# Optimization experiments

Measured on AMD Instinct MI355X. Metric: run time of the kernel, lower is better.

## Reference

```python
import jax, jax.numpy as jnp
import numpy as np

N_HEAD = 16

def setup_inputs() -> dict:
    key = jax.random.key(0)
    ks = jax.random.split(key, 5)
    B, S, C = 4, 2048, 1024
    x = jax.random.normal(ks[0], (B, S, C), dtype=jnp.float32)
    w_qkv = jax.random.normal(ks[1], (C, 3 * C), dtype=jnp.float32) * (1.0 / np.sqrt(C))
    b_qkv = jnp.zeros((3 * C,), dtype=jnp.float32)
    w_proj = jax.random.normal(ks[2], (C, C), dtype=jnp.float32) * (1.0 / np.sqrt(C))
    b_proj = jnp.zeros((C,), dtype=jnp.float32)
    return {"x": x, "w_qkv": w_qkv, "b_qkv": b_qkv, "w_proj": w_proj, "b_proj": b_proj}

def reference(x, w_qkv, b_qkv, w_proj, b_proj):
    B, S, C = x.shape
    H = N_HEAD
    D = C // H
    qkv = x @ w_qkv + b_qkv                       # [B,S,3C]
    q, k, v = jnp.split(qkv, 3, axis=-1)
    # [B,S,C] -> [B,H,S,D]
    q = q.reshape(B, S, H, D).transpose(0, 2, 1, 3)
    k = k.reshape(B, S, H, D).transpose(0, 2, 1, 3)
    v = v.reshape(B, S, H, D).transpose(0, 2, 1, 3)
    scores = jnp.einsum('bhqd,bhkd->bhqk', q, k) / jnp.sqrt(jnp.float32(D))
    causal = jnp.tril(jnp.ones((S, S), dtype=bool))
    scores = jnp.where(causal[None, None], scores, -jnp.inf)
    weights = jax.nn.softmax(scores, axis=-1)     # dropout p=0 -> identity
    out = jnp.einsum('bhqk,bhkd->bhqd', weights, v)
    out = out.transpose(0, 2, 1, 3).reshape(B, S, C)
    return out @ w_proj + b_proj
```

## Files before the change

### kernel.cpp

```cpp
#include <hip/hip_runtime.h>

#define SDIM 2048
#define CDIM 1024
#define BDIM 4
#define HDIM 16
#define DDIM 64

#define ATT_SCALE 0.18033688011112042f

typedef __attribute__((ext_vector_type(8))) short bf16x8;
typedef __attribute__((ext_vector_type(4))) short bf16x4;
typedef __attribute__((ext_vector_type(4))) float f32x4;
typedef unsigned short u16;

#define MFMA __builtin_amdgcn_mfma_f32_16x16x32_bf16
#define LDS_ORDER_FENCE() __asm__ __volatile__("" ::: "memory")

__device__ __forceinline__ u16 f2b(float f) {
    union { float f; unsigned u; } v; v.f = f;
    unsigned r = v.u + 0x7FFFu + ((v.u >> 16) & 1u);
    return (u16)(r >> 16);
}
__device__ __forceinline__ u16 f2b_trunc(float f) {
    union { float f; unsigned u; } v; v.f = f;
    return (u16)(v.u >> 16);
}

typedef const __attribute__((address_space(1))) unsigned int* gas_t;
typedef __attribute__((address_space(3))) unsigned int* las_t;
__device__ __forceinline__ void cp16(const void* g, void* l) {
    __builtin_amdgcn_global_load_lds((gas_t)g, (las_t)l, 16, 0, 0);
}

__device__ __forceinline__ float fast_exp2(float x) {
#if __has_builtin(__builtin_amdgcn_exp2f)
    return __builtin_amdgcn_exp2f(x);
#else
    return __exp2f(x);
#endif
}

__global__ __launch_bounds__(256) void prep(
    const float* __restrict__ x, const float* __restrict__ w_qkv,
    const float* __restrict__ w_proj,
    u16* __restrict__ Xb, u16* __restrict__ WqT, u16* __restrict__ WpT)
{
    __shared__ __align__(16) u16 t[64][72];
    const int bx = blockIdx.x;
    const int tid = threadIdx.x;

    if (bx < 4096) {
        int i = (bx * 256 + tid) * 8;
        float4 a = *reinterpret_cast<const float4*>(&x[i]);
        float4 b = *reinterpret_cast<const float4*>(&x[i + 4]);
        u16 u[8];
        u[0]=f2b(a.x); u[1]=f2b(a.y); u[2]=f2b(a.z); u[3]=f2b(a.w);
        u[4]=f2b(b.x); u[5]=f2b(b.y); u[6]=f2b(b.z); u[7]=f2b(b.w);
        *reinterpret_cast<uint4*>(&Xb[i]) = *reinterpret_cast<uint4*>(u);
        return;
    }

    const float* src; u16* dst; int N, n0, k0;
    if (bx < 4096 + 768) {
        int b2 = bx - 4096;
        src = w_qkv; dst = WqT; N = 3 * CDIM;
        n0 = (b2 % 48) * 64; k0 = (b2 / 48) * 64;
    } else {
        int b2 = bx - 4864;
        src = w_proj; dst = WpT; N = CDIM;
        n0 = (b2 % 16) * 64; k0 = (b2 / 16) * 64;
    }
    const int K = CDIM;
#pragma unroll
    for (int it = 0; it < 4; it++) {
        int c = tid + it * 256;
        int r = c >> 4, c4 = (c & 15) * 4;
        float4 f = *reinterpret_cast<const float4*>(&src[(size_t)(k0 + r) * N + n0 + c4]);
        t[c4 + 0][r] = f2b(f.x);
        t[c4 + 1][r] = f2b(f.y);
        t[c4 + 2][r] = f2b(f.z);
        t[c4 + 3][r] = f2b(f.w);
    }
    __syncthreads();
#pragma unroll
    for (int it = 0; it < 2; it++) {
        int c = tid + it * 256;
        int r = c >> 3, c8 = (c & 7) * 8;
        *reinterpret_cast<uint4*>(&dst[(size_t)(n0 + r) * K + k0 + c8]) =
            *reinterpret_cast<const uint4*>(&t[r][c8]);
    }
}


#define PHASE_TAIL()                                                          \
    LDS_ORDER_FENCE();                                                        \
    __builtin_amdgcn_s_barrier();                                             \
    __asm__ __volatile__("s_waitcnt lgkmcnt(0)" ::: "memory");                \
    __builtin_amdgcn_sched_barrier(0)

#define PHASE_END()                                                           \
    LDS_ORDER_FENCE();                                                        \
    __builtin_amdgcn_s_barrier()

__global__ __launch_bounds__(512, 2) void gemm_qkv(
    const u16* __restrict__ A, const u16* __restrict__ Bt,
    const float* __restrict__ bias,
    u16* __restrict__ Qb, u16* __restrict__ Kb, u16* __restrict__ Vtb)
{
    __shared__ __align__(16) u16 smem[3 * 16384 + 3 * 8192];
    u16* const AsAll = smem;
    u16* const BsAll = smem + 3 * 16384;

    const int tid = threadIdx.x, lane = tid & 63, wave = tid >> 6;
    const int wm = wave >> 1, wn = wave & 1;
    const int l16 = lane & 15, quad = lane >> 4;
    const int bid = blockIdx.x;
    const int w = (bid & 7) * 96 + (bid >> 3);
    const int bx = w % 24, by = w / 24;
    const int m0 = by * 256, n0 = bx * 128;
    const int K = CDIM;

    const int l8 = lane & 7, lr = lane >> 3;
    const int sg = l8 ^ lr;
    const int arow = wave * 8 + lr;

#define STG_A(sb, k0, s)  cp16(&A [(size_t)(m0 + (s) * 64 + arow) * K + (k0) + sg * 8], \
                               &AsAll[(sb) * 16384 + ((s) * 512 + wave * 64) * 8])
#define STG_B(sb, k0, s)  cp16(&Bt[(size_t)(n0 + (s) * 64 + arow) * K + (k0) + sg * 8], \
                               &BsAll[(sb) * 8192 + ((s) * 512 + wave * 64) * 8])
#define FRA(i, kk) (*reinterpret_cast<const bf16x8*>(                                   \
        &AsB[((wm * 64 + (i) * 16 + l16) * 8 + (((kk) * 4 + quad) ^ (l16 & 7))) * 8]))
#define FRB(j, kk) (*reinterpret_cast<const bf16x8*>(                                   \
        &BsB[((wn * 64 + (j) * 16 + l16) * 8 + (((kk) * 4 + quad) ^ (l16 & 7))) * 8]))

    f32x4 acc[4][4];
#pragma unroll
    for (int i = 0; i < 4; i++)
#pragma unroll
        for (int j = 0; j < 4; j++) acc[i][j] = (f32x4){0.f, 0.f, 0.f, 0.f};

    const int NT = K / 64;
    STG_A(0, 0, 0); STG_A(0, 0, 1); STG_A(0, 0, 2); STG_A(0, 0, 3);
    STG_B(0, 0, 0); STG_B(0, 0, 1);
    STG_A(1, 64, 0); STG_A(1, 64, 1); STG_A(1, 64, 2); STG_A(1, 64, 3);
    STG_B(1, 64, 0); STG_B(1, 64, 1);
    __asm__ __volatile__("s_waitcnt vmcnt(6)" ::: "memory");
    __builtin_amdgcn_s_barrier();
    LDS_ORDER_FENCE();

    for (int t = 0; t < NT; t++) {
        const int buf = t % 3, sbuf = (t + 2) % 3;
        const int kst = (t + 2) * 64;
        const bool st = (t + 2) < NT;
        const u16* AsB = &AsAll[buf * 16384];
        const u16* BsB = &BsAll[buf * 8192];

        bf16x8 b0, b1, b2, b3, a0, a1;

        b0 = FRB(0, 0); b1 = FRB(1, 0); b2 = FRB(2, 0); b3 = FRB(3, 0);
        a0 = FRA(0, 0); a1 = FRA(1, 0);
        if (st) { STG_A(sbuf, kst, 0); STG_A(sbuf, kst, 1); }
        PHASE_TAIL();
        __builtin_amdgcn_s_setprio(1);
        acc[0][0] = MFMA(a0, b0, acc[0][0], 0, 0, 0);
        acc[0][1] = MFMA(a0, b1, acc[0][1], 0, 0, 0);
        acc[0][2] = MFMA(a0, b2, acc[0][2], 0, 0, 0);
        acc[0][3] = MFMA(a0, b3, acc[0][3], 0, 0, 0);
        acc[1][0] = MFMA(a1, b0, acc[1][0], 0, 0, 0);
        acc[1][1] = MFMA(a1, b1, acc[1][1], 0, 0, 0);
        acc[1][2] = MFMA(a1, b2, acc[1][2], 0, 0, 0);
        acc[1][3] = MFMA(a1, b3, acc[1][3], 0, 0, 0);
        __builtin_amdgcn_s_setprio(0);
        PHASE_END();

        a0 = FRA(2, 0); a1 = FRA(3, 0);
        if (st) { STG_A(sbuf, kst, 2); STG_A(sbuf, kst, 3); }
        PHASE_TAIL();
        __builtin_amdgcn_s_setprio(1);
        acc[2][0] = MFMA(a0, b0, acc[2][0], 0, 0, 0);
        acc[2][1] = MFMA(a0, b1, acc[2][1], 0, 0, 0);
        acc[2][2] = MFMA(a0, b2, acc[2][2], 0, 0, 0);
        acc[2][3] = MFMA(a0, b3, acc[2][3], 0, 0, 0);
        acc[3][0] = MFMA(a1, b0, acc[3][0], 0, 0, 0);
        acc[3][1] = MFMA(a1, b1, acc[3][1], 0, 0, 0);
        acc[3][2] = MFMA(a1, b2, acc[3][2], 0, 0, 0);
        acc[3][3] = MFMA(a1, b3, acc[3][3], 0, 0, 0);
        __builtin_amdgcn_s_setprio(0);
        PHASE_END();

        b0 = FRB(0, 1); b1 = FRB(1, 1); b2 = FRB(2, 1); b3 = FRB(3, 1);
        a0 = FRA(0, 1); a1 = FRA(1, 1);
        if (st) { STG_B(sbuf, kst, 0); STG_B(sbuf, kst, 1); }
        PHASE_TAIL();
        __builtin_amdgcn_s_setprio(1);
        acc[0][0] = MFMA(a0, b0, acc[0][0], 0, 0, 0);
        acc[0][1] = MFMA(a0, b1, acc[0][1], 0, 0, 0);
        acc[0][2] = MFMA(a0, b2, acc[0][2], 0, 0, 0);
        acc[0][3] = MFMA(a0, b3, acc[0][3], 0, 0, 0);
        acc[1][0] = MFMA(a1, b0, acc[1][0], 0, 0, 0);
        acc[1][1] = MFMA(a1, b1, acc[1][1], 0, 0, 0);
        acc[1][2] = MFMA(a1, b2, acc[1][2], 0, 0, 0);
        acc[1][3] = MFMA(a1, b3, acc[1][3], 0, 0, 0);
        __builtin_amdgcn_s_setprio(0);
        PHASE_END();

        a0 = FRA(2, 1); a1 = FRA(3, 1);
        PHASE_TAIL();
        __builtin_amdgcn_s_setprio(1);
        acc[2][0] = MFMA(a0, b0, acc[2][0], 0, 0, 0);
        acc[2][1] = MFMA(a0, b1, acc[2][1], 0, 0, 0);
        acc[2][2] = MFMA(a0, b2, acc[2][2], 0, 0, 0);
        acc[2][3] = MFMA(a0, b3, acc[2][3], 0, 0, 0);
        acc[3][0] = MFMA(a1, b0, acc[3][0], 0, 0, 0);
        acc[3][1] = MFMA(a1, b1, acc[3][1], 0, 0, 0);
        acc[3][2] = MFMA(a1, b2, acc[3][2], 0, 0, 0);
        acc[3][3] = MFMA(a1, b3, acc[3][3], 0, 0, 0);
        __builtin_amdgcn_s_setprio(0);
        if (t < NT - 2) {
            __asm__ __volatile__("s_waitcnt vmcnt(6)" ::: "memory");
        } else if (t == NT - 2) {
            __asm__ __volatile__("s_waitcnt vmcnt(0)" ::: "memory");
        }
        PHASE_END();
    }
#undef STG_A
#undef STG_B
#undef FRA
#undef FRB

    const int mm0 = m0 + wm * 64;
    const int bidx = mm0 >> 11, s0 = mm0 & 2047;
    const int n_base = n0 + wn * 64;
    u16* eb = &smem[wave * (16 * 68)];
    const int erow = lane >> 2, ec = (lane & 3) * 16;

    if (n0 >= 2 * CDIM) {
        const int h = (n_base - 2 * CDIM) >> 6;
        const size_t gb = ((size_t)(bidx * HDIM + h)) * DDIM * SDIM;
#pragma unroll
        for (int j = 0; j < 4; j++) {
            float bvj = bias[n_base + j * 16 + l16];
            LDS_ORDER_FENCE();
#pragma unroll
            for (int i = 0; i < 4; i++)
#pragma unroll
                for (int r = 0; r < 4; r++)
                    eb[l16 * 68 + i * 16 + quad * 4 + r] = f2b(acc[i][j][r] + bvj);
            LDS_ORDER_FENCE();
            union { bf16x4 hp[4]; uint4 u[2]; } pk;
            pk.hp[0] = *reinterpret_cast<const bf16x4*>(&eb[erow * 68 + ec]);
            pk.hp[1] = *reinterpret_cast<const bf16x4*>(&eb[erow * 68 + ec + 4]);
            pk.hp[2] = *reinterpret_cast<const bf16x4*>(&eb[erow * 68 + ec + 8]);
            pk.hp[3] = *reinterpret_cast<const bf16x4*>(&eb[erow * 68 + ec + 12]);
            u16* gp = &Vtb[gb + (size_t)(j * 16 + erow) * SDIM + s0 + ec];
            *reinterpret_cast<uint4*>(gp)     = pk.u[0];
            *reinterpret_cast<uint4*>(gp + 8) = pk.u[1];
        }
    } else {
        const bool isK = (n_base >= CDIM);
        u16* dst = isK ? Kb : Qb;
        const float scale = isK ? 1.0f : ATT_SCALE;
        const int hh = (n_base & 1023) >> 6;
        const size_t hb = ((size_t)(bidx * HDIM + hh)) * SDIM;
        float bvj[4];
#pragma unroll
        for (int j = 0; j < 4; j++) bvj[j] = bias[n_base + j * 16 + l16];
#pragma unroll
        for (int i = 0; i < 4; i++) {
            LDS_ORDER_FENCE();
#pragma unroll
            for (int j = 0; j < 4; j++)
#pragma unroll
                for (int r = 0; r < 4; r++)
                    eb[(quad * 4 + r) * 68 + j * 16 + l16] =
                        f2b((acc[i][j][r] + bvj[j]) * scale);
            LDS_ORDER_FENCE();
            union { bf16x4 hp[4]; uint4 u[2]; } pk;
            pk.hp[0] = *reinterpret_cast<const bf16x4*>(&eb[erow * 68 + ec]);
            pk.hp[1] = *reinterpret_cast<const bf16x4*>(&eb[erow * 68 + ec + 4]);
            pk.hp[2] = *reinterpret_cast<const bf16x4*>(&eb[erow * 68 + ec + 8]);
            pk.hp[3] = *reinterpret_cast<const bf16x4*>(&eb[erow * 68 + ec + 12]);
            const int s = s0 + i * 16 + erow;
            u16* gp = &dst[(hb + s) * DDIM + ec];
            *reinterpret_cast<uint4*>(gp)     = pk.u[0];
            *reinterpret_cast<uint4*>(gp + 8) = pk.u[1];
        }
    }
}

__global__ __launch_bounds__(512, 6) void attn(
    const u16* __restrict__ Qb, const u16* __restrict__ Kb,
    const u16* __restrict__ Vtb, u16* __restrict__ Ob)
{
    __shared__ __align__(16) u16 Ks[2][64 * 64];
    __shared__ __align__(16) u16 Vts[2][64 * 64];
    __shared__ __align__(16) u16 Ps[8][16 * 68];

    const int tid = threadIdx.x;
    const int lane = tid & 63, wave = tid >> 6;
    const int l16 = lane & 15, quad = lane >> 4;
    const int x = blockIdx.x;
    const int bh = (x & 7) * 8 + ((x >> 3) & 7);
    const int qt = 15 - (x >> 6);
    const int q0 = qt * 128;
    const int b = bh >> 4, h = bh & 15;
    const size_t base = (size_t)bh * (SDIM * DDIM);

    const int cl0 = wave * 64 + lane;
    const int sr0 = cl0 >> 3, scc = cl0 & 7;
    const int sg0 = scc ^ (sr0 & 7);

    const int qrow = q0 + wave * 16 + l16;
    bf16x8 aq0 = *reinterpret_cast<const bf16x8*>(&Qb[base + (size_t)qrow * DDIM + quad * 8]);
    bf16x8 aq1 = *reinterpret_cast<const bf16x8*>(&Qb[base + (size_t)qrow * DDIM + 32 + quad * 8]);

    u16* Pw = &Ps[wave][0];

    f32x4 O[4];
    f32x4 Osum = (f32x4){0.f, 0.f, 0.f, 0.f};
#pragma unroll
    for (int j = 0; j < 4; j++) O[j] = (f32x4){0.f, 0.f, 0.f, 0.f};
    const short onev = (l16 == 0) ? (short)0x3F80 : (short)0;
    const bf16x8 bones = {onev, onev, onev, onev, onev, onev, onev, onev};

    const int nkb = (qt + 1) * 2;
    const int Arow = q0 + wave * 16;

    cp16(&Kb [base + (size_t)sr0 * DDIM + sg0 * 8], &Ks[0][wave * 512]);
    cp16(&Vtb[base + (size_t)sr0 * SDIM + sg0 * 8], &Vts[0][wave * 512]);

    for (int kbi = 0; kbi < nkb; kbi++) {
        const int cur = kbi & 1;
        const int kb = kbi * 64;
        __syncthreads();
        if (kbi + 1 < nkb) {
            const int kb2 = kb + 64;
            cp16(&Kb [base + (size_t)(kb2 + sr0) * DDIM + sg0 * 8], &Ks[1 - cur][wave * 512]);
            cp16(&Vtb[base + (size_t)sr0 * SDIM + kb2 + sg0 * 8], &Vts[1 - cur][wave * 512]);
        }
        if (kb > Arow + 15) continue;

        const u16* Kc = &Ks[cur][0];
        const u16* Vc = &Vts[cur][0];

        f32x4 sc[4];
#pragma unroll
        for (int j = 0; j < 4; j++) {
            int kr = j * 16 + l16;
            bf16x8 bk0 = *reinterpret_cast<const bf16x8*>(&Kc[(kr * 8 + ( quad      ^ (kr & 7))) * 8]);
            bf16x8 bk1 = *reinterpret_cast<const bf16x8*>(&Kc[(kr * 8 + ((quad + 4) ^ (kr & 7))) * 8]);
            f32x4 s = (f32x4){0.f, 0.f, 0.f, 0.f};
            s = MFMA(aq0, bk0, s, 0, 0, 0);
            s = MFMA(aq1, bk1, s, 0, 0, 0);
            sc[j] = s;
        }
        if (kb + 63 > Arow) {
            const int qrel = Arow - kb;
#pragma unroll
            for (int j = 0; j < 4; j++) {
                int kk = j * 16 + l16;
#pragma unroll
                for (int r = 0; r < 4; r++)
                    sc[j][r] = (kk <= qrel + quad * 4 + r) ? sc[j][r] : -1e30f;
            }
        }
#pragma unroll
        for (int j = 0; j < 4; j++)
#pragma unroll
            for (int r = 0; r < 4; r++) {
                float p = fast_exp2(sc[j][r]);
                Pw[(quad * 4 + r) * 68 + j * 16 + l16] = f2b_trunc(p);
            }
        LDS_ORDER_FENCE();
        union { bf16x4 hp[2]; bf16x8 f; } a0u, a1u;
        a0u.hp[0] = *reinterpret_cast<const bf16x4*>(&Pw[l16 * 68 + quad * 8]);
        a0u.hp[1] = *reinterpret_cast<const bf16x4*>(&Pw[l16 * 68 + quad * 8 + 4]);
        a1u.hp[0] = *reinterpret_cast<const bf16x4*>(&Pw[l16 * 68 + 32 + quad * 8]);
        a1u.hp[1] = *reinterpret_cast<const bf16x4*>(&Pw[l16 * 68 + 32 + quad * 8 + 4]);

#pragma unroll
        for (int j = 0; j < 4; j++) {
            int vr = j * 16 + l16;
            bf16x8 bv0 = *reinterpret_cast<const bf16x8*>(&Vc[(vr * 8 + ( quad      ^ (vr & 7))) * 8]);
            bf16x8 bv1 = *reinterpret_cast<const bf16x8*>(&Vc[(vr * 8 + ((quad + 4) ^ (vr & 7))) * 8]);
            O[j] = MFMA(a0u.f, bv0, O[j], 0, 0, 0);
            O[j] = MFMA(a1u.f, bv1, O[j], 0, 0, 0);
        }
        Osum = MFMA(a0u.f, bones, Osum, 0, 0, 0);
        Osum = MFMA(a1u.f, bones, Osum, 0, 0, 0);
    }

#pragma unroll
    for (int r = 0; r < 4; r++) {
        float l = __shfl(Osum[r], (lane & 48));
        float inv = 1.0f / l;
        int s = q0 + wave * 16 + quad * 4 + r;
#pragma unroll
        for (int j = 0; j < 4; j++)
            Ob[((size_t)(b * SDIM + s)) * CDIM + h * 64 + j * 16 + l16] =
                f2b(O[j][r] * inv);
    }
}

__global__ __launch_bounds__(512, 2) void gemm_proj(
    const u16* __restrict__ A, const u16* __restrict__ Bt,
    const float* __restrict__ bias, float* __restrict__ out)
{
    __shared__ __align__(16) u16 smem[3 * 16384 + 3 * 8192];
    u16* const AsAll = smem;
    u16* const BsAll = smem + 3 * 16384;

    const int tid = threadIdx.x, lane = tid & 63, wave = tid >> 6;
    const int wm = wave >> 1, wn = wave & 1;
    const int l16 = lane & 15, quad = lane >> 4;
    const int bid = blockIdx.x;
    const int w = (bid & 7) * 32 + (bid >> 3);
    const int bx = w & 7, by = w >> 3;
    const int m0 = by * 256, n0 = bx * 128;
    const int K = CDIM, N = CDIM;

    const int l8 = lane & 7, lr = lane >> 3;
    const int sg = l8 ^ lr;
    const int arow = wave * 8 + lr;

#define STG_A(sb, k0, s)  cp16(&A [(size_t)(m0 + (s) * 64 + arow) * K + (k0) + sg * 8], \
                               &AsAll[(sb) * 16384 + ((s) * 512 + wave * 64) * 8])
#define STG_B(sb, k0, s)  cp16(&Bt[(size_t)(n0 + (s) * 64 + arow) * K + (k0) + sg * 8], \
                               &BsAll[(sb) * 8192 + ((s) * 512 + wave * 64) * 8])
#define FRA(i, kk) (*reinterpret_cast<const bf16x8*>(                                   \
        &AsB[((wm * 64 + (i) * 16 + l16) * 8 + (((kk) * 4 + quad) ^ (l16 & 7))) * 8]))
#define FRB(j, kk) (*reinterpret_cast<const bf16x8*>(                                   \
        &BsB[((wn * 64 + (j) * 16 + l16) * 8 + (((kk) * 4 + quad) ^ (l16 & 7))) * 8]))

    f32x4 acc[4][4];
#pragma unroll
    for (int i = 0; i < 4; i++)
#pragma unroll
        for (int j = 0; j < 4; j++) acc[i][j] = (f32x4){0.f, 0.f, 0.f, 0.f};

    const int NT = K / 64;
    STG_A(0, 0, 0); STG_A(0, 0, 1); STG_A(0, 0, 2); STG_A(0, 0, 3);
    STG_B(0, 0, 0); STG_B(0, 0, 1);
    STG_A(1, 64, 0); STG_A(1, 64, 1); STG_A(1, 64, 2); STG_A(1, 64, 3);
    STG_B(1, 64, 0); STG_B(1, 64, 1);
    __asm__ __volatile__("s_waitcnt vmcnt(6)" ::: "memory");
    __builtin_amdgcn_s_barrier();
    LDS_ORDER_FENCE();

    for (int t = 0; t < NT; t++) {
        const int buf = t % 3, sbuf = (t + 2) % 3;
        const int kst = (t + 2) * 64;
        const bool st = (t + 2) < NT;
        const u16* AsB = &AsAll[buf * 16384];
        const u16* BsB = &BsAll[buf * 8192];

        bf16x8 b0, b1, b2, b3, a0, a1;

        b0 = FRB(0, 0); b1 = FRB(1, 0); b2 = FRB(2, 0); b3 = FRB(3, 0);
        a0 = FRA(0, 0); a1 = FRA(1, 0);
        if (st) { STG_A(sbuf, kst, 0); STG_A(sbuf, kst, 1); }
        PHASE_TAIL();
        __builtin_amdgcn_s_setprio(1);
        acc[0][0] = MFMA(a0, b0, acc[0][0], 0, 0, 0);
        acc[0][1] = MFMA(a0, b1, acc[0][1], 0, 0, 0);
        acc[0][2] = MFMA(a0, b2, acc[0][2], 0, 0, 0);
        acc[0][3] = MFMA(a0, b3, acc[0][3], 0, 0, 0);
        acc[1][0] = MFMA(a1, b0, acc[1][0], 0, 0, 0);
        acc[1][1] = MFMA(a1, b1, acc[1][1], 0, 0, 0);
        acc[1][2] = MFMA(a1, b2, acc[1][2], 0, 0, 0);
        acc[1][3] = MFMA(a1, b3, acc[1][3], 0, 0, 0);
        __builtin_amdgcn_s_setprio(0);
        PHASE_END();

        a0 = FRA(2, 0); a1 = FRA(3, 0);
        if (st) { STG_A(sbuf, kst, 2); STG_A(sbuf, kst, 3); }
        PHASE_TAIL();
        __builtin_amdgcn_s_setprio(1);
        acc[2][0] = MFMA(a0, b0, acc[2][0], 0, 0, 0);
        acc[2][1] = MFMA(a0, b1, acc[2][1], 0, 0, 0);
        acc[2][2] = MFMA(a0, b2, acc[2][2], 0, 0, 0);
        acc[2][3] = MFMA(a0, b3, acc[2][3], 0, 0, 0);
        acc[3][0] = MFMA(a1, b0, acc[3][0], 0, 0, 0);
        acc[3][1] = MFMA(a1, b1, acc[3][1], 0, 0, 0);
        acc[3][2] = MFMA(a1, b2, acc[3][2], 0, 0, 0);
        acc[3][3] = MFMA(a1, b3, acc[3][3], 0, 0, 0);
        __builtin_amdgcn_s_setprio(0);
        PHASE_END();

        b0 = FRB(0, 1); b1 = FRB(1, 1); b2 = FRB(2, 1); b3 = FRB(3, 1);
        a0 = FRA(0, 1); a1 = FRA(1, 1);
        if (st) { STG_B(sbuf, kst, 0); STG_B(sbuf, kst, 1); }
        PHASE_TAIL();
        __builtin_amdgcn_s_setprio(1);
        acc[0][0] = MFMA(a0, b0, acc[0][0], 0, 0, 0);
        acc[0][1] = MFMA(a0, b1, acc[0][1], 0, 0, 0);
        acc[0][2] = MFMA(a0, b2, acc[0][2], 0, 0, 0);
        acc[0][3] = MFMA(a0, b3, acc[0][3], 0, 0, 0);
        acc[1][0] = MFMA(a1, b0, acc[1][0], 0, 0, 0);
        acc[1][1] = MFMA(a1, b1, acc[1][1], 0, 0, 0);
        acc[1][2] = MFMA(a1, b2, acc[1][2], 0, 0, 0);
        acc[1][3] = MFMA(a1, b3, acc[1][3], 0, 0, 0);
        __builtin_amdgcn_s_setprio(0);
        PHASE_END();

        a0 = FRA(2, 1); a1 = FRA(3, 1);
        PHASE_TAIL();
        __builtin_amdgcn_s_setprio(1);
        acc[2][0] = MFMA(a0, b0, acc[2][0], 0, 0, 0);
        acc[2][1] = MFMA(a0, b1, acc[2][1], 0, 0, 0);
        acc[2][2] = MFMA(a0, b2, acc[2][2], 0, 0, 0);
        acc[2][3] = MFMA(a0, b3, acc[2][3], 0, 0, 0);
        acc[3][0] = MFMA(a1, b0, acc[3][0], 0, 0, 0);
        acc[3][1] = MFMA(a1, b1, acc[3][1], 0, 0, 0);
        acc[3][2] = MFMA(a1, b2, acc[3][2], 0, 0, 0);
        acc[3][3] = MFMA(a1, b3, acc[3][3], 0, 0, 0);
        __builtin_amdgcn_s_setprio(0);
        if (t < NT - 2) {
            __asm__ __volatile__("s_waitcnt vmcnt(6)" ::: "memory");
        } else if (t == NT - 2) {
            __asm__ __volatile__("s_waitcnt vmcnt(0)" ::: "memory");
        }
        PHASE_END();
    }
#undef STG_A
#undef STG_B
#undef FRA
#undef FRB

#pragma unroll
    for (int i = 0; i < 4; i++) {
        int mbase = m0 + wm * 64 + i * 16 + quad * 4;
#pragma unroll
        for (int j = 0; j < 4; j++) {
            int n = n0 + wn * 64 + j * 16 + l16;
            float bv = bias[n];
#pragma unroll
            for (int r = 0; r < 4; r++)
                out[(size_t)(mbase + r) * N + n] = acc[i][j][r] + bv;
        }
    }
}

extern "C" void kernel_launch(void* const* d_in, const int* in_sizes, int n_in,
                              void* d_out, int out_size, void* d_ws, size_t ws_size,
                              hipStream_t stream) {
    const float* x      = (const float*)d_in[0];
    const float* w_qkv  = (const float*)d_in[1];
    const float* b_qkv  = (const float*)d_in[2];
    const float* w_proj = (const float*)d_in[3];
    const float* b_proj = (const float*)d_in[4];
    float* out = (float*)d_out;

    const size_t per = (size_t)BDIM * HDIM * SDIM * DDIM;
    u16* Qb  = (u16*)d_ws;
    u16* Kb  = Qb + per;
    u16* Vtb = Kb + per;
    u16* Ob  = Vtb + per;
    u16* Xb  = Ob;
    u16* WqT = Ob + per;
    u16* WpT = WqT + (size_t)3 * CDIM * CDIM;

    prep<<<dim3(4096 + 768 + 256), dim3(256), 0, stream>>>(x, w_qkv, w_proj, Xb, WqT, WpT);

    gemm_qkv<<<dim3(768), dim3(512), 0, stream>>>(Xb, WqT, b_qkv, Qb, Kb, Vtb);
    attn<<<dim3(BDIM * HDIM * (SDIM / 128)), dim3(512), 0, stream>>>(Qb, Kb, Vtb, Ob);
    gemm_proj<<<dim3(256), dim3(512), 0, stream>>>(Ob, WpT, b_proj, out);
}
```

Before: 248.3 us.

## Restructure QKV GEMM to 4 waves with 128x64 per-wave tiles and BK=32

The QKV projection GEMM drops from 8 waves to 4 waves per block. Each wave now computes a 128x64 output tile (8x4 MFMA accumulators) instead of 64x64, and the K step shrinks from 64 to 32 with a new swizzled LDS layout and simpler fragment addressing. The aim is more register-level reuse per LDS fragment load and lower LDS use per block, which could allow more resident blocks. The cost is doubled accumulator register pressure, which may limit occupancy or cause spills, plus twice as many K iterations and barriers.

```diff
diff --git a/kernel.cpp b/kernel.cpp
--- a/kernel.cpp
+++ b/kernel.cpp
@@ -91,7 +91,6 @@
     }
 }
 
-
 #define PHASE_TAIL()                                                          \
     LDS_ORDER_FENCE();                                                        \
     __builtin_amdgcn_s_barrier();                                             \
@@ -102,14 +101,14 @@
     LDS_ORDER_FENCE();                                                        \
     __builtin_amdgcn_s_barrier()
 
-__global__ __launch_bounds__(512, 2) void gemm_qkv(
+__global__ __launch_bounds__(256, 2) void gemm_qkv(
     const u16* __restrict__ A, const u16* __restrict__ Bt,
     const float* __restrict__ bias,
     u16* __restrict__ Qb, u16* __restrict__ Kb, u16* __restrict__ Vtb)
 {
-    __shared__ __align__(16) u16 smem[3 * 16384 + 3 * 8192];
+    __shared__ __align__(16) u16 smem[3 * 8192 + 3 * 4096];
     u16* const AsAll = smem;
-    u16* const BsAll = smem + 3 * 16384;
+    u16* const BsAll = smem + 3 * 8192;
 
     const int tid = threadIdx.x, lane = tid & 63, wave = tid >> 6;
     const int wm = wave >> 1, wn = wave & 1;
@@ -119,6 +118,297 @@
     const int bx = w % 24, by = w / 24;
     const int m0 = by * 256, n0 = bx * 128;
     const int K = CDIM;
+
+    const int su = (tid & 7) ^ ((tid >> 3) & 7);
+    const int sr = ((tid >> 3) << 1) | (su >> 2);
+    const int sc = su & 3;
+
+    const int uc8 = ((((l16 & 1) << 2) | quad) ^ (l16 >> 1)) * 8;
+    const int faB = (wm * 64 + (l16 >> 1)) * 64 + uc8;
+    const int fbB = (wn * 32 + (l16 >> 1)) * 64 + uc8;
+
+#define STG_A(sb, k0, s)  cp16(&A [(size_t)(m0 + (s) * 64 + sr) * K + (k0) + sc * 8], \
+                               &AsAll[(sb) * 8192 + ((s) * 256 + wave * 64) * 8])
+#define STG_B(sb, k0, s)  cp16(&Bt[(size_t)(n0 + (s) * 64 + sr) * K + (k0) + sc * 8], \
+                               &BsAll[(sb) * 4096 + ((s) * 256 + wave * 64) * 8])
+#define FRA(i) (*reinterpret_cast<const bf16x8*>(&AsB[faB + (i) * 512]))
+#define FRB(j) (*reinterpret_cast<const bf16x8*>(&BsB[fbB + (j) * 512]))
+
+    f32x4 acc[8][4];
+#pragma unroll
+    for (int i = 0; i < 8; i++)
+#pragma unroll
+        for (int j = 0; j < 4; j++) acc[i][j] = (f32x4){0.f, 0.f, 0.f, 0.f};
+
+    const int NT = K / 32;
+    STG_A(0, 0, 0); STG_A(0, 0, 1); STG_A(0, 0, 2); STG_A(0, 0, 3);
+    STG_B(0, 0, 0); STG_B(0, 0, 1);
+    STG_A(1, 32, 0); STG_A(1, 32, 1); STG_A(1, 32, 2); STG_A(1, 32, 3);
+    STG_B(1, 32, 0); STG_B(1, 32, 1);
+    __asm__ __volatile__("s_waitcnt vmcnt(6)" ::: "memory");
+    __builtin_amdgcn_s_barrier();
+    LDS_ORDER_FENCE();
+
+    for (int t = 0; t < NT; t++) {
+        const int buf = t % 3, sbuf = (t + 2) % 3;
+        const int kst = (t + 2) * 32;
+        const bool st = (t + 2) < NT;
+        const u16* AsB = &AsAll[buf * 8192];
+        const u16* BsB = &BsAll[buf * 4096];
+
+        bf16x8 b0, b1, b2, b3, a0, a1, a2, a3;
+
+        b0 = FRB(0); b1 = FRB(1); b2 = FRB(2); b3 = FRB(3);
+        a0 = FRA(0); a1 = FRA(1); a2 = FRA(2); a3 = FRA(3);
+        if (st) { STG_A(sbuf, kst, 0); STG_A(sbuf, kst, 1); STG_A(sbuf, kst, 2); }
+        PHASE_TAIL();
+        __builtin_amdgcn_s_setprio(1);
+        acc[0][0] = MFMA(a0, b0, acc[0][0], 0, 0, 0);
+        acc[0][1] = MFMA(a0, b1, acc[0][1], 0, 0, 0);
+        acc[0][2] = MFMA(a0, b2, acc[0][2], 0, 0, 0);
+        acc[0][3] = MFMA(a0, b3, acc[0][3], 0, 0, 0);
+        acc[1][0] = MFMA(a1, b0, acc[1][0], 0, 0, 0);
+        acc[1][1] = MFMA(a1, b1, acc[1][1], 0, 0, 0);
+        acc[1][2] = MFMA(a1, b2, acc[1][2], 0, 0, 0);
+        acc[1][3] = MFMA(a1, b3, acc[1][3], 0, 0, 0);
+        acc[2][0] = MFMA(a2, b0, acc[2][0], 0, 0, 0);
+        acc[2][1] = MFMA(a2, b1, acc[2][1], 0, 0, 0);
+        acc[2][2] = MFMA(a2, b2, acc[2][2], 0, 0, 0);
+        acc[2][3] = MFMA(a2, b3, acc[2][3], 0, 0, 0);
+        acc[3][0] = MFMA(a3, b0, acc[3][0], 0, 0, 0);
+        acc[3][1] = MFMA(a3, b1, acc[3][1], 0, 0, 0);
+        acc[3][2] = MFMA(a3, b2, acc[3][2], 0, 0, 0);
+        acc[3][3] = MFMA(a3, b3, acc[3][3], 0, 0, 0);
+        __builtin_amdgcn_s_setprio(0);
+        PHASE_END();
+
+        a0 = FRA(4); a1 = FRA(5); a2 = FRA(6); a3 = FRA(7);
+        if (st) { STG_A(sbuf, kst, 3); STG_B(sbuf, kst, 0); STG_B(sbuf, kst, 1); }
+        PHASE_TAIL();
+        __builtin_amdgcn_s_setprio(1);
+        acc[4][0] = MFMA(a0, b0, acc[4][0], 0, 0, 0);
+        acc[4][1] = MFMA(a0, b1, acc[4][1], 0, 0, 0);
+        acc[4][2] = MFMA(a0, b2, acc[4][2], 0, 0, 0);
+        acc[4][3] = MFMA(a0, b3, acc[4][3], 0, 0, 0);
+        acc[5][0] = MFMA(a1, b0, acc[5][0], 0, 0, 0);
+        acc[5][1] = MFMA(a1, b1, acc[5][1], 0, 0, 0);
+        acc[5][2] = MFMA(a1, b2, acc[5][2], 0, 0, 0);
+        acc[5][3] = MFMA(a1, b3, acc[5][3], 0, 0, 0);
+        acc[6][0] = MFMA(a2, b0, acc[6][0], 0, 0, 0);
+        acc[6][1] = MFMA(a2, b1, acc[6][1], 0, 0, 0);
+        acc[6][2] = MFMA(a2, b2, acc[6][2], 0, 0, 0);
+        acc[6][3] = MFMA(a2, b3, acc[6][3], 0, 0, 0);
+        acc[7][0] = MFMA(a3, b0, acc[7][0], 0, 0, 0);
+        acc[7][1] = MFMA(a3, b1, acc[7][1], 0, 0, 0);
+        acc[7][2] = MFMA(a3, b2, acc[7][2], 0, 0, 0);
+        acc[7][3] = MFMA(a3, b3, acc[7][3], 0, 0, 0);
+        __builtin_amdgcn_s_setprio(0);
+        if (t < NT - 2) {
+            __asm__ __volatile__("s_waitcnt vmcnt(6)" ::: "memory");
+        } else if (t == NT - 2) {
+            __asm__ __volatile__("s_waitcnt vmcnt(0)" ::: "memory");
+        }
+        PHASE_END();
+    }
+#undef STG_A
+#undef STG_B
+#undef FRA
+#undef FRB
+
+    const int mm0 = m0 + wm * 128;
+    const int bidx = mm0 >> 11, s0 = mm0 & 2047;
+    const int n_base = n0 + wn * 64;
+    u16* eb = &smem[wave * (16 * 68)];
+    const int erow = lane >> 2, ec = (lane & 3) * 16;
+
+    if (n0 >= 2 * CDIM) {
+        const int h = (n_base - 2 * CDIM) >> 6;
+        const size_t gb = ((size_t)(bidx * HDIM + h)) * DDIM * SDIM;
+#pragma unroll
+        for (int ih = 0; ih < 2; ih++) {
+#pragma unroll
+            for (int j = 0; j < 4; j++) {
+                float bvj = bias[n_base + j * 16 + l16];
+                LDS_ORDER_FENCE();
+#pragma unroll
+                for (int i = 0; i < 4; i++)
+#pragma unroll
+                    for (int r = 0; r < 4; r++)
+                        eb[l16 * 68 + i * 16 + quad * 4 + r] =
+                            f2b(acc[ih * 4 + i][j][r] + bvj);
+                LDS_ORDER_FENCE();
+                union { bf16x4 hp[4]; uint4 u[2]; } pk;
+                pk.hp[0] = *reinterpret_cast<const bf16x4*>(&eb[erow * 68 + ec]);
+                pk.hp[1] = *reinterpret_cast<const bf16x4*>(&eb[erow * 68 + ec + 4]);
+                pk.hp[2] = *reinterpret_cast<const bf16x4*>(&eb[erow * 68 + ec + 8]);
+                pk.hp[3] = *reinterpret_cast<const bf16x4*>(&eb[erow * 68 + ec + 12]);
+                u16* gp = &Vtb[gb + (size_t)(j * 16 + erow) * SDIM + s0 + ih * 64 + ec];
+                *reinterpret_cast<uint4*>(gp)     = pk.u[0];
+                *reinterpret_cast<uint4*>(gp + 8) = pk.u[1];
+            }
+        }
+    } else {
+        const bool isK = (n_base >= CDIM);
+        u16* dst = isK ? Kb : Qb;
+        const float scale = isK ? 1.0f : ATT_SCALE;
+        const int hh = (n_base & 1023) >> 6;
+        const size_t hb = ((size_t)(bidx * HDIM + hh)) * SDIM;
+        float bvj[4];
+#pragma unroll
+        for (int j = 0; j < 4; j++) bvj[j] = bias[n_base + j * 16 + l16];
+#pragma unroll
+        for (int i = 0; i < 8; i++) {
+            LDS_ORDER_FENCE();
+#pragma unroll
+            for (int j = 0; j < 4; j++)
+#pragma unroll
+                for (int r = 0; r < 4; r++)
+                    eb[(quad * 4 + r) * 68 + j * 16 + l16] =
+                        f2b((acc[i][j][r] + bvj[j]) * scale);
+            LDS_ORDER_FENCE();
+            union { bf16x4 hp[4]; uint4 u[2]; } pk;
+            pk.hp[0] = *reinterpret_cast<const bf16x4*>(&eb[erow * 68 + ec]);
+            pk.hp[1] = *reinterpret_cast<const bf16x4*>(&eb[erow * 68 + ec + 4]);
+            pk.hp[2] = *reinterpret_cast<const bf16x4*>(&eb[erow * 68 + ec + 8]);
+            pk.hp[3] = *reinterpret_cast<const bf16x4*>(&eb[erow * 68 + ec + 12]);
+            const int s = s0 + i * 16 + erow;
+            u16* gp = &dst[(hb + s) * DDIM + ec];
+            *reinterpret_cast<uint4*>(gp)     = pk.u[0];
+            *reinterpret_cast<uint4*>(gp + 8) = pk.u[1];
+        }
+    }
+}
+
+__global__ __launch_bounds__(512, 6) void attn(
+    const u16* __restrict__ Qb, const u16* __restrict__ Kb,
+    const u16* __restrict__ Vtb, u16* __restrict__ Ob)
+{
+    __shared__ __align__(16) u16 Ks[2][64 * 64];
+    __shared__ __align__(16) u16 Vts[2][64 * 64];
+    __shared__ __align__(16) u16 Ps[8][16 * 68];
+
+    const int tid = threadIdx.x;
+    const int lane = tid & 63, wave = tid >> 6;
+    const int l16 = lane & 15, quad = lane >> 4;
+    const int x = blockIdx.x;
+    const int bh = (x & 7) * 8 + ((x >> 3) & 7);
+    const int qt = 15 - (x >> 6);
+    const int q0 = qt * 128;
+    const int b = bh >> 4, h = bh & 15;
+    const size_t base = (size_t)bh * (SDIM * DDIM);
+
+    const int cl0 = wave * 64 + lane;
+    const int sr0 = cl0 >> 3, scc = cl0 & 7;
+    const int sg0 = scc ^ (sr0 & 7);
+
+    const int qrow = q0 + wave * 16 + l16;
+    bf16x8 aq0 = *reinterpret_cast<const bf16x8*>(&Qb[base + (size_t)qrow * DDIM + quad * 8]);
+    bf16x8 aq1 = *reinterpret_cast<const bf16x8*>(&Qb[base + (size_t)qrow * DDIM + 32 + quad * 8]);
+
+    u16* Pw = &Ps[wave][0];
+
+    f32x4 O[4];
+    f32x4 Osum = (f32x4){0.f, 0.f, 0.f, 0.f};
+#pragma unroll
+    for (int j = 0; j < 4; j++) O[j] = (f32x4){0.f, 0.f, 0.f, 0.f};
+    const short onev = (l16 == 0) ? (short)0x3F80 : (short)0;
+    const bf16x8 bones = {onev, onev, onev, onev, onev, onev, onev, onev};
+
+    const int nkb = (qt + 1) * 2;
+    const int Arow = q0 + wave * 16;
+
+    cp16(&Kb [base + (size_t)sr0 * DDIM + sg0 * 8], &Ks[0][wave * 512]);
+    cp16(&Vtb[base + (size_t)sr0 * SDIM + sg0 * 8], &Vts[0][wave * 512]);
+
+    for (int kbi = 0; kbi < nkb; kbi++) {
+        const int cur = kbi & 1;
+        const int kb = kbi * 64;
+        __syncthreads();
+        if (kbi + 1 < nkb) {
+            const int kb2 = kb + 64;
+            cp16(&Kb [base + (size_t)(kb2 + sr0) * DDIM + sg0 * 8], &Ks[1 - cur][wave * 512]);
+            cp16(&Vtb[base + (size_t)sr0 * SDIM + kb2 + sg0 * 8], &Vts[1 - cur][wave * 512]);
+        }
+        if (kb > Arow + 15) continue;
+
+        const u16* Kc = &Ks[cur][0];
+        const u16* Vc = &Vts[cur][0];
+
+        f32x4 sc[4];
+#pragma unroll
+        for (int j = 0; j < 4; j++) {
+            int kr = j * 16 + l16;
+            bf16x8 bk0 = *reinterpret_cast<const bf16x8*>(&Kc[(kr * 8 + ( quad      ^ (kr & 7))) * 8]);
+            bf16x8 bk1 = *reinterpret_cast<const bf16x8*>(&Kc[(kr * 8 + ((quad + 4) ^ (kr & 7))) * 8]);
+            f32x4 s = (f32x4){0.f, 0.f, 0.f, 0.f};
+            s = MFMA(aq0, bk0, s, 0, 0, 0);
+            s = MFMA(aq1, bk1, s, 0, 0, 0);
+            sc[j] = s;
+        }
+        if (kb + 63 > Arow) {
+            const int qrel = Arow - kb;
+#pragma unroll
+            for (int j = 0; j < 4; j++) {
+                int kk = j * 16 + l16;
+#pragma unroll
+                for (int r = 0; r < 4; r++)
+                    sc[j][r] = (kk <= qrel + quad * 4 + r) ? sc[j][r] : -1e30f;
+            }
+        }
+#pragma unroll
+        for (int j = 0; j < 4; j++)
+#pragma unroll
+            for (int r = 0; r < 4; r++) {
+                float p = fast_exp2(sc[j][r]);
+                Pw[(quad * 4 + r) * 68 + j * 16 + l16] = f2b_trunc(p);
+            }
+        LDS_ORDER_FENCE();
+        union { bf16x4 hp[2]; bf16x8 f; } a0u, a1u;
+        a0u.hp[0] = *reinterpret_cast<const bf16x4*>(&Pw[l16 * 68 + quad * 8]);
+        a0u.hp[1] = *reinterpret_cast<const bf16x4*>(&Pw[l16 * 68 + quad * 8 + 4]);
+        a1u.hp[0] = *reinterpret_cast<const bf16x4*>(&Pw[l16 * 68 + 32 + quad * 8]);
+        a1u.hp[1] = *reinterpret_cast<const bf16x4*>(&Pw[l16 * 68 + 32 + quad * 8 + 4]);
+
+#pragma unroll
+        for (int j = 0; j < 4; j++) {
+            int vr = j * 16 + l16;
+            bf16x8 bv0 = *reinterpret_cast<const bf16x8*>(&Vc[(vr * 8 + ( quad      ^ (vr & 7))) * 8]);
+            bf16x8 bv1 = *reinterpret_cast<const bf16x8*>(&Vc[(vr * 8 + ((quad + 4) ^ (vr & 7))) * 8]);
+            O[j] = MFMA(a0u.f, bv0, O[j], 0, 0, 0);
+            O[j] = MFMA(a1u.f, bv1, O[j], 0, 0, 0);
+        }
+        Osum = MFMA(a0u.f, bones, Osum, 0, 0, 0);
+        Osum = MFMA(a1u.f, bones, Osum, 0, 0, 0);
+    }
+
+#pragma unroll
+    for (int r = 0; r < 4; r++) {
+        float l = __shfl(Osum[r], (lane & 48));
+        float inv = 1.0f / l;
+        int s = q0 + wave * 16 + quad * 4 + r;
+#pragma unroll
+        for (int j = 0; j < 4; j++)
+            Ob[((size_t)(b * SDIM + s)) * CDIM + h * 64 + j * 16 + l16] =
+                f2b(O[j][r] * inv);
+    }
+}
+
+__global__ __launch_bounds__(512, 2) void gemm_proj(
+    const u16* __restrict__ A, const u16* __restrict__ Bt,
+    const float* __restrict__ bias, float* __restrict__ out)
+{
+    __shared__ __align__(16) u16 smem[3 * 16384 + 3 * 8192];
+    u16* const AsAll = smem;
+    u16* const BsAll = smem + 3 * 16384;
+
+    const int tid = threadIdx.x, lane = tid & 63, wave = tid >> 6;
+    const int wm = wave >> 1, wn = wave & 1;
+    const int l16 = lane & 15, quad = lane >> 4;
+    const int bid = blockIdx.x;
+    const int w = (bid & 7) * 32 + (bid >> 3);
+    const int bx = w & 7, by = w >> 3;
+    const int m0 = by * 256, n0 = bx * 128;
+    const int K = CDIM, N = CDIM;
 
     const int l8 = lane & 7, lr = lane >> 3;
     const int sg = l8 ^ lr;
@@ -228,305 +518,6 @@
 #undef FRA
 #undef FRB
 
-    const int mm0 = m0 + wm * 64;
-    const int bidx = mm0 >> 11, s0 = mm0 & 2047;
-    const int n_base = n0 + wn * 64;
-    u16* eb = &smem[wave * (16 * 68)];
-    const int erow = lane >> 2, ec = (lane & 3) * 16;
-
-    if (n0 >= 2 * CDIM) {
-        const int h = (n_base - 2 * CDIM) >> 6;
-        const size_t gb = ((size_t)(bidx * HDIM + h)) * DDIM * SDIM;
-#pragma unroll
-        for (int j = 0; j < 4; j++) {
-            float bvj = bias[n_base + j * 16 + l16];
-            LDS_ORDER_FENCE();
-#pragma unroll
-            for (int i = 0; i < 4; i++)
-#pragma unroll
-                for (int r = 0; r < 4; r++)
-                    eb[l16 * 68 + i * 16 + quad * 4 + r] = f2b(acc[i][j][r] + bvj);
-            LDS_ORDER_FENCE();
-            union { bf16x4 hp[4]; uint4 u[2]; } pk;
-            pk.hp[0] = *reinterpret_cast<const bf16x4*>(&eb[erow * 68 + ec]);
-            pk.hp[1] = *reinterpret_cast<const bf16x4*>(&eb[erow * 68 + ec + 4]);
-            pk.hp[2] = *reinterpret_cast<const bf16x4*>(&eb[erow * 68 + ec + 8]);
-            pk.hp[3] = *reinterpret_cast<const bf16x4*>(&eb[erow * 68 + ec + 12]);
-            u16* gp = &Vtb[gb + (size_t)(j * 16 + erow) * SDIM + s0 + ec];
-            *reinterpret_cast<uint4*>(gp)     = pk.u[0];
-            *reinterpret_cast<uint4*>(gp + 8) = pk.u[1];
-        }
-    } else {
-        const bool isK = (n_base >= CDIM);
-        u16* dst = isK ? Kb : Qb;
-        const float scale = isK ? 1.0f : ATT_SCALE;
-        const int hh = (n_base & 1023) >> 6;
-        const size_t hb = ((size_t)(bidx * HDIM + hh)) * SDIM;
-        float bvj[4];
-#pragma unroll
-        for (int j = 0; j < 4; j++) bvj[j] = bias[n_base + j * 16 + l16];
-#pragma unroll
-        for (int i = 0; i < 4; i++) {
-            LDS_ORDER_FENCE();
-#pragma unroll
-            for (int j = 0; j < 4; j++)
-#pragma unroll
-                for (int r = 0; r < 4; r++)
-                    eb[(quad * 4 + r) * 68 + j * 16 + l16] =
-                        f2b((acc[i][j][r] + bvj[j]) * scale);
-            LDS_ORDER_FENCE();
-            union { bf16x4 hp[4]; uint4 u[2]; } pk;
-            pk.hp[0] = *reinterpret_cast<const bf16x4*>(&eb[erow * 68 + ec]);
-            pk.hp[1] = *reinterpret_cast<const bf16x4*>(&eb[erow * 68 + ec + 4]);
-            pk.hp[2] = *reinterpret_cast<const bf16x4*>(&eb[erow * 68 + ec + 8]);
-            pk.hp[3] = *reinterpret_cast<const bf16x4*>(&eb[erow * 68 + ec + 12]);
-            const int s = s0 + i * 16 + erow;
-            u16* gp = &dst[(hb + s) * DDIM + ec];
-            *reinterpret_cast<uint4*>(gp)     = pk.u[0];
-            *reinterpret_cast<uint4*>(gp + 8) = pk.u[1];
-        }
-    }
-}
-
-__global__ __launch_bounds__(512, 6) void attn(
-    const u16* __restrict__ Qb, const u16* __restrict__ Kb,
-    const u16* __restrict__ Vtb, u16* __restrict__ Ob)
-{
-    __shared__ __align__(16) u16 Ks[2][64 * 64];
-    __shared__ __align__(16) u16 Vts[2][64 * 64];
-    __shared__ __align__(16) u16 Ps[8][16 * 68];
-
-    const int tid = threadIdx.x;
-    const int lane = tid & 63, wave = tid >> 6;
-    const int l16 = lane & 15, quad = lane >> 4;
-    const int x = blockIdx.x;
-    const int bh = (x & 7) * 8 + ((x >> 3) & 7);
-    const int qt = 15 - (x >> 6);
-    const int q0 = qt * 128;
-    const int b = bh >> 4, h = bh & 15;
-    const size_t base = (size_t)bh * (SDIM * DDIM);
-
-    const int cl0 = wave * 64 + lane;
-    const int sr0 = cl0 >> 3, scc = cl0 & 7;
-    const int sg0 = scc ^ (sr0 & 7);
-
-    const int qrow = q0 + wave * 16 + l16;
-    bf16x8 aq0 = *reinterpret_cast<const bf16x8*>(&Qb[base + (size_t)qrow * DDIM + quad * 8]);
-    bf16x8 aq1 = *reinterpret_cast<const bf16x8*>(&Qb[base + (size_t)qrow * DDIM + 32 + quad * 8]);
-
-    u16* Pw = &Ps[wave][0];
-
-    f32x4 O[4];
-    f32x4 Osum = (f32x4){0.f, 0.f, 0.f, 0.f};
-#pragma unroll
-    for (int j = 0; j < 4; j++) O[j] = (f32x4){0.f, 0.f, 0.f, 0.f};
-    const short onev = (l16 == 0) ? (short)0x3F80 : (short)0;
-    const bf16x8 bones = {onev, onev, onev, onev, onev, onev, onev, onev};
-
-    const int nkb = (qt + 1) * 2;
-    const int Arow = q0 + wave * 16;
-
-    cp16(&Kb [base + (size_t)sr0 * DDIM + sg0 * 8], &Ks[0][wave * 512]);
-    cp16(&Vtb[base + (size_t)sr0 * SDIM + sg0 * 8], &Vts[0][wave * 512]);
-
-    for (int kbi = 0; kbi < nkb; kbi++) {
-        const int cur = kbi & 1;
-        const int kb = kbi * 64;
-        __syncthreads();
-        if (kbi + 1 < nkb) {
-            const int kb2 = kb + 64;
-            cp16(&Kb [base + (size_t)(kb2 + sr0) * DDIM + sg0 * 8], &Ks[1 - cur][wave * 512]);
-            cp16(&Vtb[base + (size_t)sr0 * SDIM + kb2 + sg0 * 8], &Vts[1 - cur][wave * 512]);
-        }
-        if (kb > Arow + 15) continue;
-
-        const u16* Kc = &Ks[cur][0];
-        const u16* Vc = &Vts[cur][0];
-
-        f32x4 sc[4];
-#pragma unroll
-        for (int j = 0; j < 4; j++) {
-            int kr = j * 16 + l16;
-            bf16x8 bk0 = *reinterpret_cast<const bf16x8*>(&Kc[(kr * 8 + ( quad      ^ (kr & 7))) * 8]);
-            bf16x8 bk1 = *reinterpret_cast<const bf16x8*>(&Kc[(kr * 8 + ((quad + 4) ^ (kr & 7))) * 8]);
-            f32x4 s = (f32x4){0.f, 0.f, 0.f, 0.f};
-            s = MFMA(aq0, bk0, s, 0, 0, 0);
-            s = MFMA(aq1, bk1, s, 0, 0, 0);
-            sc[j] = s;
-        }
-        if (kb + 63 > Arow) {
-            const int qrel = Arow - kb;
-#pragma unroll
-            for (int j = 0; j < 4; j++) {
-                int kk = j * 16 + l16;
-#pragma unroll
-                for (int r = 0; r < 4; r++)
-                    sc[j][r] = (kk <= qrel + quad * 4 + r) ? sc[j][r] : -1e30f;
-            }
-        }
-#pragma unroll
-        for (int j = 0; j < 4; j++)
-#pragma unroll
-            for (int r = 0; r < 4; r++) {
-                float p = fast_exp2(sc[j][r]);
-                Pw[(quad * 4 + r) * 68 + j * 16 + l16] = f2b_trunc(p);
-            }
-        LDS_ORDER_FENCE();
-        union { bf16x4 hp[2]; bf16x8 f; } a0u, a1u;
-        a0u.hp[0] = *reinterpret_cast<const bf16x4*>(&Pw[l16 * 68 + quad * 8]);
-        a0u.hp[1] = *reinterpret_cast<const bf16x4*>(&Pw[l16 * 68 + quad * 8 + 4]);
-        a1u.hp[0] = *reinterpret_cast<const bf16x4*>(&Pw[l16 * 68 + 32 + quad * 8]);
-        a1u.hp[1] = *reinterpret_cast<const bf16x4*>(&Pw[l16 * 68 + 32 + quad * 8 + 4]);
-
-#pragma unroll
-        for (int j = 0; j < 4; j++) {
-            int vr = j * 16 + l16;
-            bf16x8 bv0 = *reinterpret_cast<const bf16x8*>(&Vc[(vr * 8 + ( quad      ^ (vr & 7))) * 8]);
-            bf16x8 bv1 = *reinterpret_cast<const bf16x8*>(&Vc[(vr * 8 + ((quad + 4) ^ (vr & 7))) * 8]);
-            O[j] = MFMA(a0u.f, bv0, O[j], 0, 0, 0);
-            O[j] = MFMA(a1u.f, bv1, O[j], 0, 0, 0);
-        }
-        Osum = MFMA(a0u.f, bones, Osum, 0, 0, 0);
-        Osum = MFMA(a1u.f, bones, Osum, 0, 0, 0);
-    }
-
-#pragma unroll
-    for (int r = 0; r < 4; r++) {
-        float l = __shfl(Osum[r], (lane & 48));
-        float inv = 1.0f / l;
-        int s = q0 + wave * 16 + quad * 4 + r;
-#pragma unroll
-        for (int j = 0; j < 4; j++)
-            Ob[((size_t)(b * SDIM + s)) * CDIM + h * 64 + j * 16 + l16] =
-                f2b(O[j][r] * inv);
-    }
-}
-
-__global__ __launch_bounds__(512, 2) void gemm_proj(
-    const u16* __restrict__ A, const u16* __restrict__ Bt,
-    const float* __restrict__ bias, float* __restrict__ out)
-{
-    __shared__ __align__(16) u16 smem[3 * 16384 + 3 * 8192];
-    u16* const AsAll = smem;
-    u16* const BsAll = smem + 3 * 16384;
-
-    const int tid = threadIdx.x, lane = tid & 63, wave = tid >> 6;
-    const int wm = wave >> 1, wn = wave & 1;
-    const int l16 = lane & 15, quad = lane >> 4;
-    const int bid = blockIdx.x;
-    const int w = (bid & 7) * 32 + (bid >> 3);
-    const int bx = w & 7, by = w >> 3;
-    const int m0 = by * 256, n0 = bx * 128;
-    const int K = CDIM, N = CDIM;
-
-    const int l8 = lane & 7, lr = lane >> 3;
-    const int sg = l8 ^ lr;
-    const int arow = wave * 8 + lr;
-
-#define STG_A(sb, k0, s)  cp16(&A [(size_t)(m0 + (s) * 64 + arow) * K + (k0) + sg * 8], \
-                               &AsAll[(sb) * 16384 + ((s) * 512 + wave * 64) * 8])
-#define STG_B(sb, k0, s)  cp16(&Bt[(size_t)(n0 + (s) * 64 + arow) * K + (k0) + sg * 8], \
-                               &BsAll[(sb) * 8192 + ((s) * 512 + wave * 64) * 8])
-#define FRA(i, kk) (*reinterpret_cast<const bf16x8*>(                                   \
-        &AsB[((wm * 64 + (i) * 16 + l16) * 8 + (((kk) * 4 + quad) ^ (l16 & 7))) * 8]))
-#define FRB(j, kk) (*reinterpret_cast<const bf16x8*>(                                   \
-        &BsB[((wn * 64 + (j) * 16 + l16) * 8 + (((kk) * 4 + quad) ^ (l16 & 7))) * 8]))
-
-    f32x4 acc[4][4];
-#pragma unroll
-    for (int i = 0; i < 4; i++)
-#pragma unroll
-        for (int j = 0; j < 4; j++) acc[i][j] = (f32x4){0.f, 0.f, 0.f, 0.f};
-
-    const int NT = K / 64;
-    STG_A(0, 0, 0); STG_A(0, 0, 1); STG_A(0, 0, 2); STG_A(0, 0, 3);
-    STG_B(0, 0, 0); STG_B(0, 0, 1);
-    STG_A(1, 64, 0); STG_A(1, 64, 1); STG_A(1, 64, 2); STG_A(1, 64, 3);
-    STG_B(1, 64, 0); STG_B(1, 64, 1);
-    __asm__ __volatile__("s_waitcnt vmcnt(6)" ::: "memory");
-    __builtin_amdgcn_s_barrier();
-    LDS_ORDER_FENCE();
-
-    for (int t = 0; t < NT; t++) {
-        const int buf = t % 3, sbuf = (t + 2) % 3;
-        const int kst = (t + 2) * 64;
-        const bool st = (t + 2) < NT;
-        const u16* AsB = &AsAll[buf * 16384];
-        const u16* BsB = &BsAll[buf * 8192];
-
-        bf16x8 b0, b1, b2, b3, a0, a1;
-
-        b0 = FRB(0, 0); b1 = FRB(1, 0); b2 = FRB(2, 0); b3 = FRB(3, 0);
-        a0 = FRA(0, 0); a1 = FRA(1, 0);
-        if (st) { STG_A(sbuf, kst, 0); STG_A(sbuf, kst, 1); }
-        PHASE_TAIL();
-        __builtin_amdgcn_s_setprio(1);
-        acc[0][0] = MFMA(a0, b0, acc[0][0], 0, 0, 0);
-        acc[0][1] = MFMA(a0, b1, acc[0][1], 0, 0, 0);
-        acc[0][2] = MFMA(a0, b2, acc[0][2], 0, 0, 0);
-        acc[0][3] = MFMA(a0, b3, acc[0][3], 0, 0, 0);
-        acc[1][0] = MFMA(a1, b0, acc[1][0], 0, 0, 0);
-        acc[1][1] = MFMA(a1, b1, acc[1][1], 0, 0, 0);
-        acc[1][2] = MFMA(a1, b2, acc[1][2], 0, 0, 0);
-        acc[1][3] = MFMA(a1, b3, acc[1][3], 0, 0, 0);
-        __builtin_amdgcn_s_setprio(0);
-        PHASE_END();
-
-        a0 = FRA(2, 0); a1 = FRA(3, 0);
-        if (st) { STG_A(sbuf, kst, 2); STG_A(sbuf, kst, 3); }
-        PHASE_TAIL();
-        __builtin_amdgcn_s_setprio(1);
-        acc[2][0] = MFMA(a0, b0, acc[2][0], 0, 0, 0);
-        acc[2][1] = MFMA(a0, b1, acc[2][1], 0, 0, 0);
-        acc[2][2] = MFMA(a0, b2, acc[2][2], 0, 0, 0);
-        acc[2][3] = MFMA(a0, b3, acc[2][3], 0, 0, 0);
-        acc[3][0] = MFMA(a1, b0, acc[3][0], 0, 0, 0);
-        acc[3][1] = MFMA(a1, b1, acc[3][1], 0, 0, 0);
-        acc[3][2] = MFMA(a1, b2, acc[3][2], 0, 0, 0);
-        acc[3][3] = MFMA(a1, b3, acc[3][3], 0, 0, 0);
-        __builtin_amdgcn_s_setprio(0);
-        PHASE_END();
-
-        b0 = FRB(0, 1); b1 = FRB(1, 1); b2 = FRB(2, 1); b3 = FRB(3, 1);
-        a0 = FRA(0, 1); a1 = FRA(1, 1);
-        if (st) { STG_B(sbuf, kst, 0); STG_B(sbuf, kst, 1); }
-        PHASE_TAIL();
-        __builtin_amdgcn_s_setprio(1);
-        acc[0][0] = MFMA(a0, b0, acc[0][0], 0, 0, 0);
-        acc[0][1] = MFMA(a0, b1, acc[0][1], 0, 0, 0);
-        acc[0][2] = MFMA(a0, b2, acc[0][2], 0, 0, 0);
-        acc[0][3] = MFMA(a0, b3, acc[0][3], 0, 0, 0);
-        acc[1][0] = MFMA(a1, b0, acc[1][0], 0, 0, 0);
-        acc[1][1] = MFMA(a1, b1, acc[1][1], 0, 0, 0);
-        acc[1][2] = MFMA(a1, b2, acc[1][2], 0, 0, 0);
-        acc[1][3] = MFMA(a1, b3, acc[1][3], 0, 0, 0);
-        __builtin_amdgcn_s_setprio(0);
-        PHASE_END();
-
-        a0 = FRA(2, 1); a1 = FRA(3, 1);
-        PHASE_TAIL();
-        __builtin_amdgcn_s_setprio(1);
-        acc[2][0] = MFMA(a0, b0, acc[2][0], 0, 0, 0);
-        acc[2][1] = MFMA(a0, b1, acc[2][1], 0, 0, 0);
-        acc[2][2] = MFMA(a0, b2, acc[2][2], 0, 0, 0);
-        acc[2][3] = MFMA(a0, b3, acc[2][3], 0, 0, 0);
-        acc[3][0] = MFMA(a1, b0, acc[3][0], 0, 0, 0);
-        acc[3][1] = MFMA(a1, b1, acc[3][1], 0, 0, 0);
-        acc[3][2] = MFMA(a1, b2, acc[3][2], 0, 0, 0);
-        acc[3][3] = MFMA(a1, b3, acc[3][3], 0, 0, 0);
-        __builtin_amdgcn_s_setprio(0);
-        if (t < NT - 2) {
-            __asm__ __volatile__("s_waitcnt vmcnt(6)" ::: "memory");
-        } else if (t == NT - 2) {
-            __asm__ __volatile__("s_waitcnt vmcnt(0)" ::: "memory");
-        }
-        PHASE_END();
-    }
-#undef STG_A
-#undef STG_B
-#undef FRA
-#undef FRB
-
 #pragma unroll
     for (int i = 0; i < 4; i++) {
         int mbase = m0 + wm * 64 + i * 16 + quad * 4;
@@ -562,7 +553,7 @@
 
     prep<<<dim3(4096 + 768 + 256), dim3(256), 0, stream>>>(x, w_qkv, w_proj, Xb, WqT, WpT);
 
-    gemm_qkv<<<dim3(768), dim3(512), 0, stream>>>(Xb, WqT, b_qkv, Qb, Kb, Vtb);
+    gemm_qkv<<<dim3(768), dim3(256), 0, stream>>>(Xb, WqT, b_qkv, Qb, Kb, Vtb);
     attn<<<dim3(BDIM * HDIM * (SDIM / 128)), dim3(512), 0, stream>>>(Qb, Kb, Vtb, Ob);
     gemm_proj<<<dim3(256), dim3(512), 0, stream>>>(Ob, WpT, b_proj, out);
 }
```

New measurement: 232.7 us. -6.3%, faster.
